# Performance work log

Hardware: AMD Instinct MI355X
Metric: run time of the kernel (lower is better)

The kernel has to match this reference:

```python
import jax, jax.numpy as jnp
import numpy as np

N_ATOMS = 262144
N_SEG = 2048
DIM = 256
OUT_DIM = 256


def setup_inputs() -> dict:
    key = jax.random.key(0)
    k1, k2, k3, k4 = jax.random.split(key, 4)
    atom_features = jax.random.normal(k1, (N_ATOMS, DIM), dtype=jnp.float32)
    # ragged segment offsets: 0 = off[0] < off[1] < ... < off[S] = N_ATOMS
    rng = np.random.default_rng(0)
    interior = np.sort(rng.choice(np.arange(1, N_ATOMS), size=N_SEG - 1, replace=False))
    index_list = jnp.asarray(np.concatenate([[0], interior, [N_ATOMS]]), dtype=jnp.int64)
    # SelfAttentionPooling params: attention scorer + output projection
    Wa = jax.random.normal(k2, (DIM, 1), dtype=jnp.float32) / np.sqrt(DIM)
    ba = jnp.zeros((1,), dtype=jnp.float32)
    Wo = jax.random.normal(k3, (DIM, OUT_DIM), dtype=jnp.float32) / np.sqrt(DIM)
    bo = jnp.zeros((OUT_DIM,), dtype=jnp.float32)
    return {"atom_features": atom_features, "index_list": index_list,
            "Wa": Wa, "ba": ba, "Wo": Wo, "bo": bo}


def reference(atom_features, index_list, Wa, ba, Wo, bo):
    S = index_list.shape[0] - 1          # number of segments (static)
    N = atom_features.shape[0]
    # segment id of each atom from the offsets vector
    seg = jnp.searchsorted(index_list, jnp.arange(N), side="right") - 1  # [N]
    # per-atom attention logits
    logits = (atom_features @ Wa + ba)[:, 0]                             # [N]
    # segment-wise stable softmax
    seg_max = jax.ops.segment_max(logits, seg, num_segments=S)           # [S]
    e = jnp.exp(logits - seg_max[seg])                                   # [N]
    denom = jax.ops.segment_sum(e, seg, num_segments=S)                  # [S]
    att = e / denom[seg]                                                 # [N]
    # attention-weighted pooling per segment
    pooled = jax.ops.segment_sum(att[:, None] * atom_features, seg, num_segments=S)  # [S, DIM]
    return pooled @ Wo + bo                                              # [S, OUT_DIM]
```

## Files before the change

kernel.cpp:

```cpp
#include <hip/hip_runtime.h>

#define DIM 256
#define NSEG 2048
#define NATOMS 262144
#define TA 8
#define NTILES (NATOMS / TA)
#define SLOTS (NSEG + NTILES)
#define WPB 4

__device__ __forceinline__ long long load_off(const void* p, int i, int is64) {
  if (is64) return ((const long long*)p)[i];
  return (long long)((const int*)p)[i];
}

__device__ __forceinline__ float wave_sum_b(float v) {
  int x;
  x = __builtin_amdgcn_update_dpp(0, __float_as_int(v), 0xB1, 0xF, 0xF, true);
  v += __int_as_float(x);
  x = __builtin_amdgcn_update_dpp(0, __float_as_int(v), 0x4E, 0xF, 0xF, true);
  v += __int_as_float(x);
  x = __builtin_amdgcn_update_dpp(0, __float_as_int(v), 0x141, 0xF, 0xF, true);
  v += __int_as_float(x);
  x = __builtin_amdgcn_update_dpp(0, __float_as_int(v), 0x140, 0xF, 0xF, true);
  v += __int_as_float(x);
  v += __int_as_float(__builtin_amdgcn_ds_swizzle(__float_as_int(v), 0x401F));
  v += __shfl_xor(v, 32);
  return v;
}

__device__ __forceinline__ unsigned bf16rne(float f) {
  unsigned u = __float_as_uint(f);
  return (u + 0x7FFFu + ((u >> 16) & 1u)) >> 16;
}
__device__ __forceinline__ unsigned pack2(float a, float b) {
  return bf16rne(a) | (bf16rne(b) << 16);
}
__device__ __forceinline__ float4 unpack4(uint2 u) {
  float4 f;
  f.x = __uint_as_float(u.x << 16);
  f.y = __uint_as_float(u.x & 0xFFFF0000u);
  f.z = __uint_as_float(u.y << 16);
  f.w = __uint_as_float(u.y & 0xFFFF0000u);
  return f;
}

__global__ void seg_of_tile(const void* __restrict__ offs_raw,
                            int* __restrict__ s0tab,
                            int* __restrict__ s1tab)
{
  int s = blockIdx.x * blockDim.x + threadIdx.x;
  if (s >= NSEG) return;
  const int is64 = (((const int*)offs_raw)[1] == 0);
  const int lo = (int)load_off(offs_raw, s, is64);
  const int hi = (int)load_off(offs_raw, s + 1, is64);
  {
    int u0 = (lo + TA - 1) / TA;
    int u1 = (hi + TA - 1) / TA - 1;
    for (int u = u0; u <= u1; ++u) s0tab[u] = s;
  }
  {
    int u0 = lo / TA;
    int u1 = hi >= TA ? (hi - TA) / TA : -1;
    for (int u = u0; u <= u1; ++u) s1tab[u] = s;
  }
}

__global__ __launch_bounds__(256, 4)
void pool_waves(const float* __restrict__ feat,
                const void* __restrict__ offs_raw,
                const float* __restrict__ Wa,
                const int* __restrict__ s0tab,
                const int* __restrict__ s1tab,
                float* __restrict__ md,
                uint2* __restrict__ accbuf)
{
  const int lane = threadIdx.x & 63;
  const int wv   = threadIdx.x >> 6;
  const int u    = blockIdx.x * WPB + wv;
  const int base = u * TA;
  const int is64 = (((const int*)offs_raw)[1] == 0);

  const float4* fg = (const float4*)feat + (size_t)base * (DIM / 4);

  float4 r[TA];
#pragma unroll
  for (int k = 0; k < TA; ++k) r[k] = fg[(size_t)k * 64 + lane];

  const int s0 = s0tab[u];
  const int s1 = s1tab[u];
  const float4 wa4 = ((const float4*)Wa)[lane];

  float lg[TA];
#pragma unroll
  for (int k = 0; k < TA; ++k) {
    float p = r[k].x * wa4.x + r[k].y * wa4.y + r[k].z * wa4.z + r[k].w * wa4.w;
    lg[k] = wave_sum_b(p);
  }

  if (s0 == s1) {
    float m = lg[0];
#pragma unroll
    for (int k = 1; k < TA; ++k) m = fmaxf(m, lg[k]);
    float d = 0.f;
    float4 acc = make_float4(0.f, 0.f, 0.f, 0.f);
#pragma unroll
    for (int k = 0; k < TA; ++k) {
      float e = __expf(lg[k] - m);
      d += e;
      acc.x = fmaf(e, r[k].x, acc.x);
      acc.y = fmaf(e, r[k].y, acc.y);
      acc.z = fmaf(e, r[k].z, acc.z);
      acc.w = fmaf(e, r[k].w, acc.w);
    }
    const int slot = s0 + u;
    accbuf[(size_t)slot * 64 + lane] = make_uint2(pack2(acc.x, acc.y),
                                                  pack2(acc.z, acc.w));
    if (lane == 0) *((float2*)(md + 2 * slot)) = make_float2(m, d);
  } else {
    for (int s = s0; s <= s1; ++s) {
      int lo = (int)load_off(offs_raw, s, is64);
      int hi = (int)load_off(offs_raw, s + 1, is64);
      int la = lo - base; la = la > 0 ? la : 0;
      int lb = hi - base; lb = lb < TA ? lb : TA;
      float m = -INFINITY;
#pragma unroll
      for (int k = 0; k < TA; ++k)
        if (k >= la && k < lb) m = fmaxf(m, lg[k]);
      float d = 0.f;
      float4 acc = make_float4(0.f, 0.f, 0.f, 0.f);
#pragma unroll
      for (int k = 0; k < TA; ++k) {
        bool v = (k >= la && k < lb);
        float e = v ? __expf(lg[k] - m) : 0.f;
        d += e;
        acc.x = fmaf(e, r[k].x, acc.x);
        acc.y = fmaf(e, r[k].y, acc.y);
        acc.z = fmaf(e, r[k].z, acc.z);
        acc.w = fmaf(e, r[k].w, acc.w);
      }
      const int slot = s + u;
      accbuf[(size_t)slot * 64 + lane] = make_uint2(pack2(acc.x, acc.y),
                                                    pack2(acc.z, acc.w));
      if (lane == 0) *((float2*)(md + 2 * slot)) = make_float2(m, d);
    }
  }
}

__global__ __launch_bounds__(256, 4)
void merge_project(const float* __restrict__ md,
                   const uint2* __restrict__ accbuf,
                   const void* __restrict__ offs_raw,
                   const float* __restrict__ Wo,
                   const float* __restrict__ bo,
                   float* __restrict__ out)
{
  __shared__ float pooled[4][DIM];
  __shared__ float sc_s[4][64];
  const int tid  = threadIdx.x;
  const int lane = tid & 63;
  const int wv   = tid >> 6;
  const int is64 = (((const int*)offs_raw)[1] == 0);
  const int s    = blockIdx.x * 4 + wv;

  {
    const int lo = (int)load_off(offs_raw, s, is64);
    const int hi = (int)load_off(offs_raw, s + 1, is64);
    const int u0 = lo / TA;
    const int u1 = (hi - 1) / TA;
    const int n  = u1 - u0 + 1;

    float M = -INFINITY, D = 0.f;
    float4 acc = make_float4(0.f, 0.f, 0.f, 0.f);

    for (int c0 = 0; c0 < n; c0 += 64) {
      const int j = c0 + lane;
      const bool v = (j < n);
      const int slot = s + u0 + j;
      float mj = v ? md[2 * slot] : -INFINITY;
      float dj = v ? md[2 * slot + 1] : 0.f;

      float Mc = mj;
      Mc = fmaxf(Mc, __shfl_xor(Mc, 32));
      Mc = fmaxf(Mc, __shfl_xor(Mc, 16));
      Mc = fmaxf(Mc, __shfl_xor(Mc, 8));
      Mc = fmaxf(Mc, __shfl_xor(Mc, 4));
      Mc = fmaxf(Mc, __shfl_xor(Mc, 2));
      Mc = fmaxf(Mc, __shfl_xor(Mc, 1));
      const float Mn = fmaxf(M, Mc);
      const float rs = (c0 == 0) ? 0.f : __expf(M - Mn);
      const float scj = __expf(mj - Mn);

      float t = dj * scj;
      t += __shfl_xor(t, 32);
      t += __shfl_xor(t, 16);
      t += __shfl_xor(t, 8);
      t += __shfl_xor(t, 4);
      t += __shfl_xor(t, 2);
      t += __shfl_xor(t, 1);
      D = D * rs + t;

      sc_s[wv][lane] = scj;

      acc.x *= rs; acc.y *= rs; acc.z *= rs; acc.w *= rs;

      const int cn = (n - c0) < 64 ? (n - c0) : 64;
      const uint2* ab = accbuf + (size_t)(s + u0 + c0) * 64;
      int jj = 0;
      for (; jj + 4 <= cn; jj += 4) {
        float4 a0 = unpack4(ab[(size_t)(jj + 0) * 64 + lane]);
        float4 a1 = unpack4(ab[(size_t)(jj + 1) * 64 + lane]);
        float4 a2 = unpack4(ab[(size_t)(jj + 2) * 64 + lane]);
        float4 a3 = unpack4(ab[(size_t)(jj + 3) * 64 + lane]);
        float s0 = sc_s[wv][jj + 0], s1 = sc_s[wv][jj + 1];
        float s2 = sc_s[wv][jj + 2], s3 = sc_s[wv][jj + 3];
        acc.x = fmaf(s0, a0.x, fmaf(s1, a1.x, fmaf(s2, a2.x, fmaf(s3, a3.x, acc.x))));
        acc.y = fmaf(s0, a0.y, fmaf(s1, a1.y, fmaf(s2, a2.y, fmaf(s3, a3.y, acc.y))));
        acc.z = fmaf(s0, a0.z, fmaf(s1, a1.z, fmaf(s2, a2.z, fmaf(s3, a3.z, acc.z))));
        acc.w = fmaf(s0, a0.w, fmaf(s1, a1.w, fmaf(s2, a2.w, fmaf(s3, a3.w, acc.w))));
      }
      for (; jj < cn; ++jj) {
        float4 a0 = unpack4(ab[(size_t)jj * 64 + lane]);
        float s0 = sc_s[wv][jj];
        acc.x = fmaf(s0, a0.x, acc.x);
        acc.y = fmaf(s0, a0.y, acc.y);
        acc.z = fmaf(s0, a0.z, acc.z);
        acc.w = fmaf(s0, a0.w, acc.w);
      }
      M = Mn;
    }

    const float inv = 1.f / D;
    ((float4*)pooled[wv])[lane] =
        make_float4(acc.x * inv, acc.y * inv, acc.z * inv, acc.w * inv);
  }
  __syncthreads();

  float o0 = 0.f, o1 = 0.f, o2 = 0.f, o3 = 0.f;
  for (int k = 0; k < DIM; ++k) {
    float w = Wo[k * DIM + tid];
    o0 = fmaf(pooled[0][k], w, o0);
    o1 = fmaf(pooled[1][k], w, o1);
    o2 = fmaf(pooled[2][k], w, o2);
    o3 = fmaf(pooled[3][k], w, o3);
  }
  const float b = bo[tid];
  const int sb = blockIdx.x * 4;
  out[(size_t)(sb + 0) * DIM + tid] = o0 + b;
  out[(size_t)(sb + 1) * DIM + tid] = o1 + b;
  out[(size_t)(sb + 2) * DIM + tid] = o2 + b;
  out[(size_t)(sb + 3) * DIM + tid] = o3 + b;
}

extern "C" void kernel_launch(void* const* d_in, const int* in_sizes, int n_in,
                              void* d_out, int out_size, void* d_ws, size_t ws_size,
                              hipStream_t stream)
{
  const float* feat = (const float*)d_in[0];
  const void*  offs = d_in[1];
  const float* Wa   = (const float*)d_in[2];
  const float* Wo   = (const float*)d_in[4];
  const float* bo   = (const float*)d_in[5];
  float* out = (float*)d_out;

  float* md     = (float*)d_ws;
  uint2* accbuf = (uint2*)(md + 2 * SLOTS);
  int*   s0tab  = (int*)(accbuf + (size_t)SLOTS * 64);
  int*   s1tab  = s0tab + NTILES;

  hipLaunchKernelGGL(seg_of_tile, dim3((NSEG + 255) / 256), dim3(256), 0, stream,
                     offs, s0tab, s1tab);
  hipLaunchKernelGGL(pool_waves, dim3(NTILES / WPB), dim3(256), 0, stream,
                     feat, offs, Wa, s0tab, s1tab, md, accbuf);
  hipLaunchKernelGGL(merge_project, dim3(NSEG / 4), dim3(256), 0, stream,
                     md, accbuf, offs, Wo, bo, out);
}
```

Measured before the change: 77.67 us.

## Process 32 atoms per wave with double-buffered loads and online softmax

Each wave now handles 32 atoms in four sub-tiles of 8, double-buffering feature loads across two register sets so the next sub-tile's loads overlap the current one's compute. Per-segment state is carried with an online-softmax rescale, and a partial slot is flushed only when a segment boundary is crossed. This cuts the number of partial slots, the accbuf traffic and the work in the merge kernel, and it quarters the grid. The cost is more registers per wave, a serial per-atom path with extra exps in boundary sub-tiles, and fewer waves in flight.

```diff
diff --git a/kernel.cpp b/kernel.cpp
--- a/kernel.cpp
+++ b/kernel.cpp
@@ -3,10 +3,13 @@
 #define DIM 256
 #define NSEG 2048
 #define NATOMS 262144
-#define TA 8
+#define SUB 8
+#define NSUB 4
+#define TA (SUB * NSUB)
 #define NTILES (NATOMS / TA)
 #define SLOTS (NSEG + NTILES)
 #define WPB 4
+#define NBLK (NTILES / WPB)
 
 __device__ __forceinline__ long long load_off(const void* p, int i, int is64) {
   if (is64) return ((const long long*)p)[i];
@@ -82,68 +85,89 @@
 
   const float4* fg = (const float4*)feat + (size_t)base * (DIM / 4);
 
-  float4 r[TA];
+  float4 A[SUB], B[SUB];
 #pragma unroll
-  for (int k = 0; k < TA; ++k) r[k] = fg[(size_t)k * 64 + lane];
-
-  const int s0 = s0tab[u];
-  const int s1 = s1tab[u];
+  for (int k = 0; k < SUB; ++k) A[k] = fg[(size_t)k * 64 + lane];
+#pragma unroll
+  for (int k = 0; k < SUB; ++k) B[k] = fg[(size_t)(SUB + k) * 64 + lane];
+
+  int s_cur = s0tab[u];
+  const int s_end = s1tab[u];
   const float4 wa4 = ((const float4*)Wa)[lane];
-
-  float lg[TA];
+  int hi_cur = (int)load_off(offs_raw, s_cur + 1, is64);
+
+  float m = -INFINITY, d = 0.f;
+  float4 acc = make_float4(0.f, 0.f, 0.f, 0.f);
+
+#define FLUSH_PART() do {                                                  \
+    const int slot_ = s_cur + u;              \
+    accbuf[(size_t)slot_ * 64 + lane] =                                    \
+        make_uint2(pack2(acc.x, acc.y), pack2(acc.z, acc.w));              \
+    if (lane == 0) *((float2*)(md + 2 * slot_)) = make_float2(m, d);       \
+  } while (0)
+
+#define PROC_SUB(R, t) do {                                                \
+    float lg[SUB];                                                         \
+    _Pragma("unroll")                                                      \
+    for (int k = 0; k < SUB; ++k) {                                        \
+      float p = R[k].x * wa4.x + R[k].y * wa4.y +                          \
+                R[k].z * wa4.z + R[k].w * wa4.w;                           \
+      lg[k] = wave_sum_b(p);                                               \
+    }                                                                      \
+    if (s_cur == s_end) {                   \
+      float mt = lg[0];                                                    \
+      _Pragma("unroll")                                                    \
+      for (int k = 1; k < SUB; ++k) mt = fmaxf(mt, lg[k]);                 \
+      const float mn = fmaxf(m, mt);                                       \
+      const float sc = __expf(m - mn);                    \
+      d *= sc;                                                             \
+      acc.x *= sc; acc.y *= sc; acc.z *= sc; acc.w *= sc;                  \
+      _Pragma("unroll")                                                    \
+      for (int k = 0; k < SUB; ++k) {                                      \
+        float e = __expf(lg[k] - mn);                                      \
+        d += e;                                                            \
+        acc.x = fmaf(e, R[k].x, acc.x);                                    \
+        acc.y = fmaf(e, R[k].y, acc.y);                                    \
+        acc.z = fmaf(e, R[k].z, acc.z);                                    \
+        acc.w = fmaf(e, R[k].w, acc.w);                                    \
+      }                                                                    \
+      m = mn;                                                              \
+    } else {                                \
+      _Pragma("unroll")                                                    \
+      for (int k = 0; k < SUB; ++k) {                                      \
+        const int a = base + (t) * SUB + k;              \
+        if (a >= hi_cur) {                  \
+          FLUSH_PART();                                                    \
+          m = -INFINITY; d = 0.f;                                          \
+          acc = make_float4(0.f, 0.f, 0.f, 0.f);                           \
+          s_cur += 1;                                                      \
+          hi_cur = (int)load_off(offs_raw, s_cur + 1, is64);               \
+        }                                                                  \
+        const float mn = fmaxf(m, lg[k]);                                  \
+        const float sc = __expf(m - mn);                                   \
+        const float e  = __expf(lg[k] - mn);                               \
+        d = fmaf(d, sc, e);                                                \
+        acc.x = fmaf(acc.x, sc, e * R[k].x);                               \
+        acc.y = fmaf(acc.y, sc, e * R[k].y);                               \
+        acc.z = fmaf(acc.z, sc, e * R[k].z);                               \
+        acc.w = fmaf(acc.w, sc, e * R[k].w);                               \
+        m = mn;                                                            \
+      }                                                                    \
+    }                                                                      \
+  } while (0)
+
+  PROC_SUB(A, 0);
 #pragma unroll
-  for (int k = 0; k < TA; ++k) {
-    float p = r[k].x * wa4.x + r[k].y * wa4.y + r[k].z * wa4.z + r[k].w * wa4.w;
-    lg[k] = wave_sum_b(p);
-  }
-
-  if (s0 == s1) {
-    float m = lg[0];
+  for (int k = 0; k < SUB; ++k) A[k] = fg[(size_t)(2 * SUB + k) * 64 + lane];
+  PROC_SUB(B, 1);
 #pragma unroll
-    for (int k = 1; k < TA; ++k) m = fmaxf(m, lg[k]);
-    float d = 0.f;
-    float4 acc = make_float4(0.f, 0.f, 0.f, 0.f);
-#pragma unroll
-    for (int k = 0; k < TA; ++k) {
-      float e = __expf(lg[k] - m);
-      d += e;
-      acc.x = fmaf(e, r[k].x, acc.x);
-      acc.y = fmaf(e, r[k].y, acc.y);
-      acc.z = fmaf(e, r[k].z, acc.z);
-      acc.w = fmaf(e, r[k].w, acc.w);
-    }
-    const int slot = s0 + u;
-    accbuf[(size_t)slot * 64 + lane] = make_uint2(pack2(acc.x, acc.y),
-                                                  pack2(acc.z, acc.w));
-    if (lane == 0) *((float2*)(md + 2 * slot)) = make_float2(m, d);
-  } else {
-    for (int s = s0; s <= s1; ++s) {
-      int lo = (int)load_off(offs_raw, s, is64);
-      int hi = (int)load_off(offs_raw, s + 1, is64);
-      int la = lo - base; la = la > 0 ? la : 0;
-      int lb = hi - base; lb = lb < TA ? lb : TA;
-      float m = -INFINITY;
-#pragma unroll
-      for (int k = 0; k < TA; ++k)
-        if (k >= la && k < lb) m = fmaxf(m, lg[k]);
-      float d = 0.f;
-      float4 acc = make_float4(0.f, 0.f, 0.f, 0.f);
-#pragma unroll
-      for (int k = 0; k < TA; ++k) {
-        bool v = (k >= la && k < lb);
-        float e = v ? __expf(lg[k] - m) : 0.f;
-        d += e;
-        acc.x = fmaf(e, r[k].x, acc.x);
-        acc.y = fmaf(e, r[k].y, acc.y);
-        acc.z = fmaf(e, r[k].z, acc.z);
-        acc.w = fmaf(e, r[k].w, acc.w);
-      }
-      const int slot = s + u;
-      accbuf[(size_t)slot * 64 + lane] = make_uint2(pack2(acc.x, acc.y),
-                                                    pack2(acc.z, acc.w));
-      if (lane == 0) *((float2*)(md + 2 * slot)) = make_float2(m, d);
-    }
-  }
+  for (int k = 0; k < SUB; ++k) B[k] = fg[(size_t)(3 * SUB + k) * 64 + lane];
+  PROC_SUB(A, 2);
+  PROC_SUB(B, 3);
+
+  FLUSH_PART();
+#undef PROC_SUB
+#undef FLUSH_PART
 }
 
 __global__ __launch_bounds__(256, 4)
@@ -269,7 +293,7 @@
 
   hipLaunchKernelGGL(seg_of_tile, dim3((NSEG + 255) / 256), dim3(256), 0, stream,
                      offs, s0tab, s1tab);
-  hipLaunchKernelGGL(pool_waves, dim3(NTILES / WPB), dim3(256), 0, stream,
+  hipLaunchKernelGGL(pool_waves, dim3(NBLK), dim3(256), 0, stream,
                      feat, offs, Wa, s0tab, s1tab, md, accbuf);
   hipLaunchKernelGGL(merge_project, dim3(NSEG / 4), dim3(256), 0, stream,
                      md, accbuf, offs, Wo, bo, out);
```

Result: faster. 66.52 us, median of 2 (-14.4%).
